# Kernel tuning notes

Hardware: AMD Instinct MI355X
Metric: run time of the kernel (lower is better)

## Reference

```python
import jax, jax.numpy as jnp
import numpy as np
import math

B, S, D, H = 8, 1024, 512, 8  # batch, seqlen, d_model, heads
DK = D // H

def setup_inputs() -> dict:
    key = jax.random.key(0)
    ks = jax.random.split(key, 8)
    std = 1.0 / math.sqrt(D)
    return {
        "x": jax.random.normal(ks[0], (B, S, D), jnp.float32),
        "utT_similarities": jax.random.uniform(ks[1], (B, S, S), jnp.float32),
        "Wk": jax.random.normal(ks[2], (D, D), jnp.float32) * std,
        "bk": jnp.zeros((D,), jnp.float32),
        "Wv": jax.random.normal(ks[3], (D, D), jnp.float32) * std,
        "bv": jnp.zeros((D,), jnp.float32),
        "Wo": jax.random.normal(ks[4], (D, D), jnp.float32) * std,
        "bo": jnp.zeros((D,), jnp.float32),
        "gammas": jax.random.normal(ks[5], (H, 1, 1), jnp.float32) * 0.1,
    }

def reference(x, utT_similarities, Wk, bk, Wv, bv, Wo, bo, gammas):
    b, s, d = x.shape
    h = gammas.shape[0]
    dk = d // h
    NEG = -1e32

    def split_heads(t):  # [b,s,d] -> [b,h,s,dk]
        return t.reshape(b, s, h, dk).transpose(0, 2, 1, 3)

    # kq_same=True: q and k share k_linear
    q = split_heads(x @ Wk.T + bk)
    k = q
    v = split_heads(x @ Wv.T + bv)

    scores = jnp.einsum('bhid,bhjd->bhij', q, k) / jnp.sqrt(jnp.float32(dk))
    scores = scores * utT_similarities[:, None, :, :]

    mask = jnp.tril(jnp.ones((s, s), dtype=bool))  # causal, incl diagonal (mask=1)

    # distance-decay block (no_grad in torch -> stop_gradient)
    s_ = jax.nn.softmax(jnp.where(mask, scores, NEG), axis=-1) * mask
    distcum = jnp.cumsum(s_, axis=-1)
    disttotal = jnp.sum(s_, axis=-1, keepdims=True)
    idx = jnp.arange(s)
    position_effect = jnp.abs(idx[None, :] - idx[:, None]).astype(jnp.float32)  # [s,s]
    dist_scores = jnp.sqrt(jnp.clip((disttotal - distcum) * position_effect, 0.0, None))
    dist_scores = jax.lax.stop_gradient(dist_scores)

    gamma = -jax.nn.softplus(gammas)[None]  # [1,h,1,1]
    total_effect = jnp.clip(jnp.exp(dist_scores * gamma), 1e-5, 1e5)

    scores = jax.nn.softmax(jnp.where(mask, scores * total_effect, NEG), axis=-1)
    # zero_pad=False (mask=1 path), dropout is identity in eval
    out = jnp.einsum('bhij,bhjd->bhid', scores, v)
    out = out.transpose(0, 2, 1, 3).reshape(b, s, d)
    return out @ Wo.T + bo
```

## Files before the change

kernel.cpp:

```cpp
#include <hip/hip_runtime.h>
#include <math.h>

#define NB   8
#define SS   1024
#define DD   512
#define HH   8
#define DKK  64
#define NEGF (-3.0e38f)
#define SC   (0.125f * 1.4426950408889634f)

#define QSTR 88
#define SSTR 257
#define PSTR 280

typedef _Float16 half8 __attribute__((ext_vector_type(8)));
typedef float    f32x4 __attribute__((ext_vector_type(4)));

#define GLDS16(g, l) __builtin_amdgcn_global_load_lds( \
    (const __attribute__((address_space(1))) void*)(g), \
    (__attribute__((address_space(3))) void*)(l), 16, 0, 0)

template<int CTRL, int RM, int BM, bool BC>
__device__ __forceinline__ float dpp_f(float x) {
    return __builtin_bit_cast(float,
        __builtin_amdgcn_update_dpp(0, __builtin_bit_cast(int, x),
                                    CTRL, RM, BM, BC));
}

__device__ __forceinline__ float scan64(float x) {
    x += dpp_f<0x111, 0xf, 0xf, true >(x);
    x += dpp_f<0x112, 0xf, 0xf, true >(x);
    x += dpp_f<0x114, 0xf, 0xf, true >(x);
    x += dpp_f<0x118, 0xf, 0xf, true >(x);
    x += dpp_f<0x142, 0xa, 0xf, false>(x);
    x += dpp_f<0x143, 0xc, 0xf, false>(x);
    return x;
}

__device__ __forceinline__ float redsum64(float x) {
    x += dpp_f<0xB1,  0xf, 0xf, true>(x);
    x += dpp_f<0x4E,  0xf, 0xf, true>(x);
    x += dpp_f<0x141, 0xf, 0xf, true>(x);
    x += dpp_f<0x140, 0xf, 0xf, true>(x);
    x += __shfl_xor(x, 16);
    x += __shfl_xor(x, 32);
    return x;
}

__device__ __forceinline__ float bcast63(float x) {
    return __builtin_bit_cast(float,
        __builtin_amdgcn_readlane(__builtin_bit_cast(int, x), 63));
}

__global__ __launch_bounds__(256) void cvt_fp16(
    const float* __restrict__ x,  _Float16* __restrict__ xh,
    const float* __restrict__ wk, _Float16* __restrict__ wkh,
    const float* __restrict__ wv, _Float16* __restrict__ wvh,
    const float* __restrict__ wo, _Float16* __restrict__ woh)
{
    const size_t NX = (size_t)NB * SS * DD;
    const size_t NW = (size_t)DD * DD;
    size_t f = ((size_t)blockIdx.x * 256 + threadIdx.x) * 8;
    const float* src; _Float16* dst; size_t off;
    if (f < NX)               { src = x;  dst = xh;  off = f; }
    else if (f < NX + NW)     { src = wk; dst = wkh; off = f - NX; }
    else if (f < NX + 2*NW)   { src = wv; dst = wvh; off = f - NX - 2*NW + NW; }
    else                      { src = wo; dst = woh; off = f - NX - 2*NW; }
    float4 f0 = *(const float4*)&src[off];
    float4 f1 = *(const float4*)&src[off + 4];
    half8 hv = {(_Float16)f0.x,(_Float16)f0.y,(_Float16)f0.z,(_Float16)f0.w,
                (_Float16)f1.x,(_Float16)f1.y,(_Float16)f1.z,(_Float16)f1.w};
    *(half8*)&dst[off] = hv;
}

__global__ __launch_bounds__(256) void gemm_qv(
    const _Float16* __restrict__ xh,
    const _Float16* __restrict__ wkh, const float* __restrict__ bk,
    const _Float16* __restrict__ wvh, const float* __restrict__ bv,
    _Float16* __restrict__ q_ws, _Float16* __restrict__ vt_ws)
{
    __shared__ __align__(16) _Float16 Ah[128 * 32];
    __shared__ __align__(16) _Float16 Bh[128 * 32];

    const int m0  = blockIdx.x * 128;
    const int n0c = blockIdx.y * 128;
    const bool is_v = (n0c >= DD);
    const _Float16* __restrict__ Wp = is_v ? wvh : wkh;
    const float*    __restrict__ bp = is_v ? bv : bk;
    const int n0 = n0c & (DD - 1);

    const int tid  = threadIdx.x;
    const int w    = tid >> 6;
    const int lane = tid & 63;
    const int quad = lane >> 4;
    const int n    = lane & 15;
    const int wm   = w >> 1, wn = w & 1;

    const int ci0 = (w * 2 + 0) * 64 + lane;
    const int ci1 = (w * 2 + 1) * 64 + lane;
    const int r0c = ci0 >> 2, c0c = (ci0 & 3) * 8;
    const int r1c = ci1 >> 2, c1c = (ci1 & 3) * 8;
    _Float16* ldsA0 = &Ah[(w * 2 + 0) * 512];
    _Float16* ldsA1 = &Ah[(w * 2 + 1) * 512];
    _Float16* ldsB0 = &Bh[(w * 2 + 0) * 512];
    _Float16* ldsB1 = &Bh[(w * 2 + 1) * 512];

    f32x4 acc[4][4] = {};

    for (int k0 = 0; k0 < DD; k0 += 32) {
        __syncthreads();
        GLDS16(&xh[(size_t)(m0 + r0c) * DD + k0 + c0c], ldsA0);
        GLDS16(&xh[(size_t)(m0 + r1c) * DD + k0 + c1c], ldsA1);
        GLDS16(&Wp[(size_t)(n0 + r0c) * DD + k0 + c0c], ldsB0);
        GLDS16(&Wp[(size_t)(n0 + r1c) * DD + k0 + c1c], ldsB1);
        __syncthreads();
        half8 af[4], bf[4];
        #pragma unroll
        for (int mi = 0; mi < 4; ++mi)
            af[mi] = *(const half8*)&Ah[(wm*64 + mi*16 + n) * 32 + quad*8];
        #pragma unroll
        for (int ni = 0; ni < 4; ++ni)
            bf[ni] = *(const half8*)&Bh[(wn*64 + ni*16 + n) * 32 + quad*8];
        #pragma unroll
        for (int mi = 0; mi < 4; ++mi)
            #pragma unroll
            for (int ni = 0; ni < 4; ++ni)
                acc[mi][ni] = __builtin_amdgcn_mfma_f32_16x16x32_f16(
                    af[mi], bf[ni], acc[mi][ni], 0, 0, 0);
    }

    #pragma unroll
    for (int mi = 0; mi < 4; ++mi) {
        #pragma unroll
        for (int ni = 0; ni < 4; ++ni) {
            const int col = n0 + wn*64 + ni*16 + n;
            const int h   = col >> 6;
            const int dk  = col & 63;
            const float bias = bp[col];
            const int gbase = m0 + wm*64 + mi*16 + quad*4;
            const int bidx  = gbase >> 10;
            const int sr    = gbase & (SS - 1);
            if (!is_v) {
                #pragma unroll
                for (int reg = 0; reg < 4; ++reg)
                    q_ws[((size_t)(bidx * HH + h) * SS + sr + reg) * DKK + dk] =
                        (_Float16)(acc[mi][ni][reg] + bias);
            } else {
                _Float16 h4[4];
                #pragma unroll
                for (int reg = 0; reg < 4; ++reg)
                    h4[reg] = (_Float16)(acc[mi][ni][reg] + bias);
                *(uint2*)&vt_ws[((size_t)(bidx * HH + h) * DKK + dk) * SS + sr] =
                    *(uint2*)h4;
            }
        }
    }
}

__global__ __launch_bounds__(256) void gemm_out(
    const _Float16* __restrict__ A,
    const _Float16* __restrict__ woh, const float* __restrict__ bo,
    float* __restrict__ out)
{
    __shared__ __align__(16) _Float16 Ah[128 * 32];
    __shared__ __align__(16) _Float16 Bh[128 * 32];

    const int m0 = blockIdx.x * 128;
    const int n0 = blockIdx.y * 128;

    const int tid  = threadIdx.x;
    const int w    = tid >> 6;
    const int lane = tid & 63;
    const int quad = lane >> 4;
    const int n    = lane & 15;
    const int wm   = w >> 1, wn = w & 1;

    const int ci0 = (w * 2 + 0) * 64 + lane;
    const int ci1 = (w * 2 + 1) * 64 + lane;
    const int r0c = ci0 >> 2, c0c = (ci0 & 3) * 8;
    const int r1c = ci1 >> 2, c1c = (ci1 & 3) * 8;
    _Float16* ldsA0 = &Ah[(w * 2 + 0) * 512];
    _Float16* ldsA1 = &Ah[(w * 2 + 1) * 512];
    _Float16* ldsB0 = &Bh[(w * 2 + 0) * 512];
    _Float16* ldsB1 = &Bh[(w * 2 + 1) * 512];

    f32x4 acc[4][4] = {};

    for (int k0 = 0; k0 < DD; k0 += 32) {
        __syncthreads();
        GLDS16(&A[(size_t)(m0 + r0c) * DD + k0 + c0c], ldsA0);
        GLDS16(&A[(size_t)(m0 + r1c) * DD + k0 + c1c], ldsA1);
        GLDS16(&woh[(size_t)(n0 + r0c) * DD + k0 + c0c], ldsB0);
        GLDS16(&woh[(size_t)(n0 + r1c) * DD + k0 + c1c], ldsB1);
        __syncthreads();
        half8 af[4], bf[4];
        #pragma unroll
        for (int mi = 0; mi < 4; ++mi)
            af[mi] = *(const half8*)&Ah[(wm*64 + mi*16 + n) * 32 + quad*8];
        #pragma unroll
        for (int ni = 0; ni < 4; ++ni)
            bf[ni] = *(const half8*)&Bh[(wn*64 + ni*16 + n) * 32 + quad*8];
        #pragma unroll
        for (int mi = 0; mi < 4; ++mi)
            #pragma unroll
            for (int ni = 0; ni < 4; ++ni)
                acc[mi][ni] = __builtin_amdgcn_mfma_f32_16x16x32_f16(
                    af[mi], bf[ni], acc[mi][ni], 0, 0, 0);
    }

    #pragma unroll
    for (int mi = 0; mi < 4; ++mi) {
        #pragma unroll
        for (int ni = 0; ni < 4; ++ni) {
            const int col  = n0 + wn*64 + ni*16 + n;
            const float bias = bo[col];
            const int gbase = m0 + wm*64 + mi*16 + quad*4;
            #pragma unroll
            for (int reg = 0; reg < 4; ++reg)
                out[(size_t)(gbase + reg) * DD + col] = acc[mi][ni][reg] + bias;
        }
    }
}

__global__ __launch_bounds__(1024, 8) void attn_mfma(
    const _Float16* __restrict__ q,
    const _Float16* __restrict__ vt,
    const float* __restrict__ utT,
    const float* __restrict__ gammas,
    _Float16* __restrict__ attn)
{
    __shared__ __align__(16) unsigned char smem[4 * 16 * PSTR * 2];
    __shared__ __align__(16) _Float16 q_lds[16 * QSTR];
    float*    s_lds = (float*)smem;
    _Float16* p_lds = (_Float16*)smem;

    const int tid  = threadIdx.x;
    const int w    = tid >> 6;
    const int lane = tid & 63;
    const int quad = lane >> 4;
    const int n    = lane & 15;
    const int bh   = blockIdx.y;
    const int b    = bh >> 3;
    const int h    = bh & 7;
    const int r0   = ((SS / 16 - 1) - blockIdx.x) * 16;

    const _Float16* __restrict__ kq  = q  + (size_t)bh * SS * DKK;
    const _Float16* __restrict__ vtp = vt + (size_t)bh * DKK * SS;

    const int nchunk = (r0 + 16 + 255) >> 8;
    const int nt     = nchunk * 4;

    if (tid < 256) {
        const int row = tid >> 4;
        const int c   = tid & 15;
        *(uint2*)&q_lds[row * QSTR + c * 4] =
            *(const uint2*)&kq[(size_t)(r0 + row) * DKK + c * 4];
    }
    __syncthreads();

    float sreg[16];
    #pragma unroll
    for (int t2 = 0; t2 < 16; ++t2) sreg[t2] = NEGF;

    #pragma unroll
    for (int c0 = 0; c0 < 4; ++c0) {
        if (c0 < nchunk) {
            const int j0  = c0 * 256;
            const int buf = (c0 & 1) * 16 * SSTR;
            const int jbase = j0 + w * 16;
            if (jbase <= r0 + 15) {
                const _Float16* krow = &kq[(size_t)(jbase + n) * DKK];
                half8 b0 = *(const half8*)&krow[quad * 8];
                half8 b1 = *(const half8*)&krow[32 + quad * 8];
                half8 a0 = *(const half8*)&q_lds[n * QSTR + quad * 8];
                half8 a1 = *(const half8*)&q_lds[n * QSTR + 32 + quad * 8];
                f32x4 d = {0.f, 0.f, 0.f, 0.f};
                d = __builtin_amdgcn_mfma_f32_16x16x32_f16(a0, b0, d, 0, 0, 0);
                d = __builtin_amdgcn_mfma_f32_16x16x32_f16(a1, b1, d, 0, 0, 0);
                const int j = jbase + n;
                #pragma unroll
                for (int reg = 0; reg < 4; ++reg) {
                    const int i = r0 + quad * 4 + reg;
                    float val = NEGF;
                    if (j <= i)
                        val = d[reg] * SC * utT[((size_t)b * SS + i) * SS + j];
                    s_lds[buf + (quad * 4 + reg) * SSTR + w * 16 + n] = val;
                }
            } else {
                #pragma unroll
                for (int reg = 0; reg < 4; ++reg)
                    s_lds[buf + (quad * 4 + reg) * SSTR + w * 16 + n] = NEGF;
            }
            __syncthreads();
            #pragma unroll
            for (int ttl = 0; ttl < 4; ++ttl)
                sreg[c0 * 4 + ttl] = s_lds[buf + w * SSTR + ttl * 64 + lane];
        }
    }

    const int i_row = r0 + w;
    const int ntw_u = (i_row >> 6) + 1;
    const int ntw   = (nt < ntw_u) ? nt : ntw_u;

    float cs[16];
    float carry = 0.f;
    #pragma unroll
    for (int t2 = 0; t2 < 16; ++t2) {
        if (t2 < ntw) {
            const float e  = __builtin_amdgcn_exp2f(sreg[t2]);
            const float xv = scan64(e);
            cs[t2] = carry + xv;
            carry += bcast63(xv);
        }
    }
    const float z1     = carry;
    const float inv_z1 = 1.0f / z1;

    const float g     = gammas[h];
    const float gl2   = -log1pf(__expf(g)) * 1.4426950408889634f;
    const float flane = (float)lane;

    float z2 = 0.f;
    #pragma unroll
    for (int t2 = 0; t2 < 16; ++t2) {
        if (t2 < ntw) {
            const float pe = (float)(i_row - t2 * 64) - flane;
            const float dd = fmaxf((z1 - cs[t2]) * pe, 0.0f) * inv_z1;
            float te = __builtin_amdgcn_exp2f(__builtin_amdgcn_sqrtf(dd) * gl2);
            te = fmaxf(te, 1e-5f);
            const float p = __builtin_amdgcn_exp2f(sreg[t2] * te);
            sreg[t2] = p;
            z2 += p;
        } else {
            sreg[t2] = 0.f;
        }
    }
    z2 = redsum64(z2);
    const float inv_z2 = 1.0f / z2;

    __syncthreads();

    #pragma unroll
    for (int c0 = 0; c0 < 4; ++c0) {
        if (c0 < nchunk) {
            #pragma unroll
            for (int ttl = 0; ttl < 4; ++ttl)
                p_lds[c0 * 16 * PSTR + w * PSTR + ttl * 64 + lane] =
                    (_Float16)(sreg[c0 * 4 + ttl] * inv_z2);
        }
    }

    const int KT = (r0 + 16 + 31) >> 5;
    const _Float16* vrow = &vtp[(size_t)(w * 16 + n) * SS];
    half8 vb[4] = {};
    if (w < 4) {
        #pragma unroll
        for (int u = 0; u < 4; ++u)
            if (u < KT) vb[u] = *(const half8*)&vrow[u * 32 + quad * 8];
    }
    __syncthreads();

    f32x4 oacc = {0.f, 0.f, 0.f, 0.f};
    if (w < 4) {
        for (int kt0 = 0; kt0 < KT; kt0 += 4) {
            half8 cur[4];
            #pragma unroll
            for (int u = 0; u < 4; ++u) cur[u] = vb[u];
            #pragma unroll
            for (int u = 0; u < 4; ++u) {
                const int k = kt0 + 4 + u;
                if (k < KT) vb[u] = *(const half8*)&vrow[k * 32 + quad * 8];
            }
            #pragma unroll
            for (int u = 0; u < 4; ++u) {
                const int k = kt0 + u;
                if (k < KT) {
                    half8 a = *(const half8*)&p_lds[((k >> 3) * 16 + n) * PSTR +
                                                    (k & 7) * 32 + quad * 8];
                    oacc = __builtin_amdgcn_mfma_f32_16x16x32_f16(
                        a, cur[u], oacc, 0, 0, 0);
                }
            }
        }
        #pragma unroll
        for (int reg = 0; reg < 4; ++reg) {
            const int i = r0 + quad * 4 + reg;
            attn[(((size_t)b * SS + i) * HH + h) * DKK + w * 16 + n] =
                (_Float16)oacc[reg];
        }
    }
}

extern "C" void kernel_launch(void* const* d_in, const int* in_sizes, int n_in,
                              void* d_out, int out_size, void* d_ws, size_t ws_size,
                              hipStream_t stream) {
    const float* x      = (const float*)d_in[0];
    const float* utT    = (const float*)d_in[1];
    const float* Wk     = (const float*)d_in[2];
    const float* bk     = (const float*)d_in[3];
    const float* Wv     = (const float*)d_in[4];
    const float* bv     = (const float*)d_in[5];
    const float* Wo     = (const float*)d_in[6];
    const float* bo     = (const float*)d_in[7];
    const float* gammas = (const float*)d_in[8];
    float* out = (float*)d_out;

    const size_t NX  = (size_t)NB * SS * DD;
    const size_t NW  = (size_t)DD * DD;
    const size_t per = NX;

    _Float16* p      = (_Float16*)d_ws;
    _Float16* xh     = p;  p += NX;
    _Float16* wkh    = p;  p += NW;
    _Float16* wvh    = p;  p += NW;
    _Float16* woh    = p;  p += NW;
    _Float16* q_ws   = p;  p += per;
    _Float16* vt_ws  = p;  p += per;
    _Float16* attn_h = p;  p += per;

    const int cvt_blocks = (int)((NX + 3 * NW) / 8 / 256);
    cvt_fp16<<<cvt_blocks, dim3(256), 0, stream>>>(
        x, xh, Wk, wkh, Wv, wvh, Wo, woh);

    dim3 g1(64, 8);
    gemm_qv<<<g1, dim3(256), 0, stream>>>(xh, wkh, bk, wvh, bv, q_ws, vt_ws);

    dim3 g2(SS / 16, NB * HH);
    attn_mfma<<<g2, dim3(1024), 0, stream>>>(q_ws, vt_ws, utT, gammas, attn_h);

    dim3 g3(64, 4);
    gemm_out<<<g3, dim3(256), 0, stream>>>(attn_h, woh, bo, out);
}
```

Before: 290.9 us.

## Prefetch K and similarity tiles, transpose score MFMA, use raw LDS-only barriers

The score phase now issues the K-row and utT loads for the next 256-column chunk before computing the current one, so global latency overlaps the MFMA and barrier. The MFMA operands are swapped so each lane holds four contiguous columns of one row. That lets utT be fetched as one 16-byte vector load and the scores written to LDS as a single float4, with SSTR padded to keep those stores aligned. Full __syncthreads are replaced by a barrier that waits only on lgkmcnt, so outstanding global loads are not drained at each sync. The launch-bounds occupancy hint is dropped, and relying on lgkmcnt alone is a correctness risk if any global writes feed LDS consumers.

```diff
diff --git a/kernel.cpp b/kernel.cpp
--- a/kernel.cpp
+++ b/kernel.cpp
@@ -10,7 +10,7 @@
 #define SC   (0.125f * 1.4426950408889634f)
 
 #define QSTR 88
-#define SSTR 257
+#define SSTR 260
 #define PSTR 280
 
 typedef _Float16 half8 __attribute__((ext_vector_type(8)));
@@ -19,6 +19,13 @@
 #define GLDS16(g, l) __builtin_amdgcn_global_load_lds( \
     (const __attribute__((address_space(1))) void*)(g), \
     (__attribute__((address_space(3))) void*)(l), 16, 0, 0)
+
+#define RAW_BARRIER() do {                                   \
+    __builtin_amdgcn_sched_barrier(0);                       \
+    asm volatile("s_waitcnt lgkmcnt(0)" ::: "memory");       \
+    __builtin_amdgcn_s_barrier();                            \
+    __builtin_amdgcn_sched_barrier(0);                       \
+} while (0)
 
 template<int CTRL, int RM, int BM, bool BC>
 __device__ __forceinline__ float dpp_f(float x) {
@@ -222,7 +229,7 @@
     }
 }
 
-__global__ __launch_bounds__(1024, 8) void attn_mfma(
+__global__ __launch_bounds__(1024) void attn_mfma(
     const _Float16* __restrict__ q,
     const _Float16* __restrict__ vt,
     const float* __restrict__ utT,
@@ -250,48 +257,71 @@
     const int nchunk = (r0 + 16 + 255) >> 8;
     const int nt     = nchunk * 4;
 
+    const int i_lane = r0 + n;
+
+    half8 kb0c, kb1c; f32x4 utc;
+    {
+        const int jb0 = w * 16;
+        if (jb0 <= r0 + 15) {
+            const _Float16* krow = &kq[(size_t)(jb0 + n) * DKK];
+            kb0c = *(const half8*)&krow[quad * 8];
+            kb1c = *(const half8*)&krow[32 + quad * 8];
+            utc  = *(const f32x4*)&utT[((size_t)b * SS + i_lane) * SS + jb0 + quad * 4];
+        }
+    }
+
     if (tid < 256) {
         const int row = tid >> 4;
         const int c   = tid & 15;
         *(uint2*)&q_lds[row * QSTR + c * 4] =
             *(const uint2*)&kq[(size_t)(r0 + row) * DKK + c * 4];
     }
-    __syncthreads();
+    RAW_BARRIER();
+
+    const half8 qa0 = *(const half8*)&q_lds[n * QSTR + quad * 8];
+    const half8 qa1 = *(const half8*)&q_lds[n * QSTR + 32 + quad * 8];
 
     float sreg[16];
-    #pragma unroll
-    for (int t2 = 0; t2 < 16; ++t2) sreg[t2] = NEGF;
 
     #pragma unroll
     for (int c0 = 0; c0 < 4; ++c0) {
         if (c0 < nchunk) {
-            const int j0  = c0 * 256;
-            const int buf = (c0 & 1) * 16 * SSTR;
+            const int j0    = c0 * 256;
+            const int buf   = (c0 & 1) * 16 * SSTR;
             const int jbase = j0 + w * 16;
-            if (jbase <= r0 + 15) {
-                const _Float16* krow = &kq[(size_t)(jbase + n) * DKK];
-                half8 b0 = *(const half8*)&krow[quad * 8];
-                half8 b1 = *(const half8*)&krow[32 + quad * 8];
-                half8 a0 = *(const half8*)&q_lds[n * QSTR + quad * 8];
-                half8 a1 = *(const half8*)&q_lds[n * QSTR + 32 + quad * 8];
+            const bool act  = (jbase <= r0 + 15);
+
+            const half8 k0 = kb0c, k1 = kb1c;
+            const f32x4 ut = utc;
+
+            if (c0 + 1 < nchunk) {
+                const int jbn = j0 + 256 + w * 16;
+                if (jbn <= r0 + 15) {
+                    const _Float16* krn = &kq[(size_t)(jbn + n) * DKK];
+                    kb0c = *(const half8*)&krn[quad * 8];
+                    kb1c = *(const half8*)&krn[32 + quad * 8];
+                    utc  = *(const f32x4*)&utT[((size_t)b * SS + i_lane) * SS
+                                               + jbn + quad * 4];
+                }
+            }
+
+            f32x4 v;
+            if (act) {
                 f32x4 d = {0.f, 0.f, 0.f, 0.f};
-                d = __builtin_amdgcn_mfma_f32_16x16x32_f16(a0, b0, d, 0, 0, 0);
-                d = __builtin_amdgcn_mfma_f32_16x16x32_f16(a1, b1, d, 0, 0, 0);
-                const int j = jbase + n;
+                d = __builtin_amdgcn_mfma_f32_16x16x32_f16(k0, qa0, d, 0, 0, 0);
+                d = __builtin_amdgcn_mfma_f32_16x16x32_f16(k1, qa1, d, 0, 0, 0);
                 #pragma unroll
                 for (int reg = 0; reg < 4; ++reg) {
-                    const int i = r0 + quad * 4 + reg;
-                    float val = NEGF;
-                    if (j <= i)
-                        val = d[reg] * SC * utT[((size_t)b * SS + i) * SS + j];
-                    s_lds[buf + (quad * 4 + reg) * SSTR + w * 16 + n] = val;
+                    const int j = jbase + quad * 4 + reg;
+                    v[reg] = (j <= i_lane) ? d[reg] * SC * ut[reg] : NEGF;
                 }
             } else {
-                #pragma unroll
-                for (int reg = 0; reg < 4; ++reg)
-                    s_lds[buf + (quad * 4 + reg) * SSTR + w * 16 + n] = NEGF;
+                v = (f32x4){NEGF, NEGF, NEGF, NEGF};
             }
-            __syncthreads();
+            *(f32x4*)&s_lds[buf + n * SSTR + w * 16 + quad * 4] = v;
+
+            RAW_BARRIER();
+
             #pragma unroll
             for (int ttl = 0; ttl < 4; ++ttl)
                 sreg[c0 * 4 + ttl] = s_lds[buf + w * SSTR + ttl * 64 + lane];
@@ -338,7 +368,7 @@
     z2 = redsum64(z2);
     const float inv_z2 = 1.0f / z2;
 
-    __syncthreads();
+    RAW_BARRIER();
 
     #pragma unroll
     for (int c0 = 0; c0 < 4; ++c0) {
@@ -358,7 +388,7 @@
         for (int u = 0; u < 4; ++u)
             if (u < KT) vb[u] = *(const half8*)&vrow[u * 32 + quad * 8];
     }
-    __syncthreads();
+    RAW_BARRIER();
 
     f32x4 oacc = {0.f, 0.f, 0.f, 0.f};
     if (w < 4) {
```

Measured after the change: 317.1 us. +9.0%, slower.
